# Kernel optimization log

Hardware: AMD Instinct MI355X
Metric: run time of the kernel (lower is better)

The kernel has to match this reference:

```python
import jax, jax.numpy as jnp
import numpy as np

N_NODES = 65536   # N
D_HID   = 128     # D (hidden)
N_GROUPS = 16384  # G portfolios
GROUP_LEN = 64    # lines per portfolio (port_len entries)
N_LINES = N_GROUPS * GROUP_LEN  # L
BATCH = 16384     # B samples


def setup_inputs() -> dict:
    key = jax.random.key(0)
    k = jax.random.split(key, 5)
    H = jax.random.normal(k[0], (N_NODES, D_HID), dtype=jnp.float32)
    port_w_signed_flat = jax.random.normal(k[1], (N_LINES,), dtype=jnp.float32)
    anchor_idx = jax.random.randint(k[2], (BATCH,), 0, N_NODES, dtype=jnp.int32)
    pf_gid = jax.random.randint(k[3], (BATCH,), 0, N_GROUPS, dtype=jnp.int32)
    port_nodes_flat = jax.random.randint(k[4], (N_LINES,), 0, N_NODES, dtype=jnp.int32)
    port_len = jnp.full((N_GROUPS,), GROUP_LEN, dtype=jnp.int32)
    return {
        'H': H,
        'port_w_signed_flat': port_w_signed_flat,
        'anchor_idx': anchor_idx,
        'pf_gid': pf_gid,
        'port_nodes_flat': port_nodes_flat,
        'port_len': port_len,
    }


def reference(H, port_w_signed_flat, anchor_idx, pf_gid, port_nodes_flat, port_len):
    """Faithful, vectorized port of compute_samplewise_portfolio_vectors_loo.

    Ragged segment-weighted mean per portfolio group, with strict leave-one-out
    correction for each sample's anchor node, followed by L2 normalization.
    Returns (V_abs, V_sgn), each [B, D].
    """
    N, D = H.shape
    G = port_len.shape[0]
    L = port_nodes_flat.shape[0]

    # gid per flat line: repeat_interleave(arange(G), lens)
    gid_lines = jnp.repeat(jnp.arange(G, dtype=jnp.int32), port_len,
                           total_repeat_length=L)

    w_abs = jnp.abs(port_w_signed_flat)
    Hl = H[port_nodes_flat]                                  # [L, D] gather
    S_abs = jax.ops.segment_sum(w_abs[:, None] * Hl, gid_lines, num_segments=G)
    W_abs = jax.ops.segment_sum(w_abs, gid_lines, num_segments=G)
    W_sgn = jax.ops.segment_sum(port_w_signed_flat, gid_lines, num_segments=G)

    valid = (pf_gid >= 0) & (pf_gid < G)
    g = jnp.clip(pf_gid, 0, G - 1)

    # Leave-one-out self-weight: sum of w over lines where (gid==g_i, node==anchor_i).
    # Vectorized join via a sorted composite int32 key (G*N < 2^31 by construction).
    keys_l = gid_lines * N + port_nodes_flat                 # [L]
    keys_s = g * N + anchor_idx                              # [B]
    order = jnp.argsort(keys_l)
    sk = keys_l[order]
    zero1 = jnp.zeros((1,), H.dtype)
    ca = jnp.concatenate([zero1, jnp.cumsum(w_abs[order])])
    cs = jnp.concatenate([zero1, jnp.cumsum(port_w_signed_flat[order])])
    lo = jnp.searchsorted(sk, keys_s, side='left')
    hi = jnp.searchsorted(sk, keys_s, side='right')
    self_w_abs = ca[hi] - ca[lo]                             # [B]
    self_w_sgn = cs[hi] - cs[lo]                             # [B]

    Ha = H[anchor_idx]                                       # [B, D]
    denom = jnp.maximum(W_abs[g] - self_w_abs, 1e-12)        # clamp_min
    V_abs = (S_abs[g] - self_w_abs[:, None] * Ha) / denom[:, None]
    V_sgn = ((W_sgn[g] - self_w_sgn) / denom)[:, None] * V_abs

    V_abs = jnp.where(valid[:, None], V_abs, jnp.zeros((), H.dtype))
    V_sgn = jnp.where(valid[:, None], V_sgn, jnp.zeros((), H.dtype))

    # torch F.normalize: x / clamp(||x||, min=eps)
    na = jnp.linalg.norm(V_abs, axis=1, keepdims=True)
    V_abs = V_abs / jnp.maximum(na, 1e-6)
    ns = jnp.linalg.norm(V_sgn, axis=1, keepdims=True)
    V_sgn = jnp.where(ns > 0, V_sgn / jnp.maximum(ns, 1e-6), V_sgn)
    return V_abs, V_sgn
```

## Files before the change

### kernel.cpp

```cpp
#include <hip/hip_runtime.h>
#include <hip/hip_bf16.h>


__global__ __launch_bounds__(1024) void scan_offsets_kernel(
    const int* __restrict__ len, int* __restrict__ offs, int G) {
    __shared__ int part[1024];
    const int t = threadIdx.x;
    const int chunk = (G + 1023) >> 10;
    const int lo = min(t * chunk, G);
    const int hi = min(lo + chunk, G);
    int s = 0;
    for (int i = lo; i < hi; ++i) s += len[i];
    part[t] = s;
    __syncthreads();
    #pragma unroll
    for (int ofs = 1; ofs < 1024; ofs <<= 1) {
        int v = (t >= ofs) ? part[t - ofs] : 0;
        __syncthreads();
        part[t] += v;
        __syncthreads();
    }
    int run = part[t] - s;
    for (int i = lo; i < hi; ++i) { offs[i] = run; run += len[i]; }
}

__global__ __launch_bounds__(256) void pf_loo_kernel(
    const float* __restrict__ H,
    const float* __restrict__ pw,
    const int* __restrict__ anchor_idx,
    const int* __restrict__ pf_gid,
    const int* __restrict__ pn,
    const int* __restrict__ plen,
    const int* __restrict__ offs,
    float* __restrict__ out,
    int B, int G) {
    const int b = blockIdx.x * (blockDim.x >> 6) + (threadIdx.x >> 6);
    const int lane = threadIdx.x & 63;
    const int half = lane >> 5;
    const int qlane = lane & 31;
    if (b >= B) return;

    float4* outA = (float4*)(out + (size_t)b * 128);
    float4* outS = (float4*)(out + ((size_t)B + b) * 128);

    const int gid = pf_gid[b];
    if (!(gid >= 0 && gid < G)) {
        float4 z = make_float4(0.f, 0.f, 0.f, 0.f);
        if (half == 0) { outA[qlane] = z; outS[qlane] = z; }
        return;
    }

    const int anchor = anchor_idx[b];
    const int off = offs[gid];
    const int len = plen[gid];

    float4 acc = make_float4(0.f, 0.f, 0.f, 0.f);
    float laWa = 0.f, laWs = 0.f, laSa = 0.f, laSs = 0.f;

    for (int base = 0; base < len; base += 64) {
        const int jmax = min(64, len - base);
        float wl = 0.f;
        int nl = 0;
        if (lane < jmax) {
            wl = pw[off + base + lane];
            nl = pn[off + base + lane];
        }
        const float wla = fabsf(wl);
        laWa += wla;
        laWs += wl;
        if (nl == anchor && lane < jmax) { laSa += wla; laSs += wl; }

        #pragma unroll 8
        for (int jj = 0; jj < 64; jj += 2) {
            const float w0 = __shfl(wl, jj);
            const float w1 = __shfl(wl, jj + 1);
            const int n0 = __shfl(nl, jj);
            const int n1 = __shfl(nl, jj + 1);
            const int row = half ? n1 : n0;
            const float ww = fabsf(half ? w1 : w0);
            const float4 h = ((const float4*)(H + (size_t)row * 128))[qlane];
            acc.x = fmaf(ww, h.x, acc.x);
            acc.y = fmaf(ww, h.y, acc.y);
            acc.z = fmaf(ww, h.z, acc.z);
            acc.w = fmaf(ww, h.w, acc.w);
        }
    }

    #pragma unroll
    for (int m = 32; m; m >>= 1) {
        laWa += __shfl_xor(laWa, m);
        laWs += __shfl_xor(laWs, m);
        laSa += __shfl_xor(laSa, m);
        laSs += __shfl_xor(laSs, m);
    }
    acc.x += __shfl_xor(acc.x, 32);
    acc.y += __shfl_xor(acc.y, 32);
    acc.z += __shfl_xor(acc.z, 32);
    acc.w += __shfl_xor(acc.w, 32);

    const float denom = fmaxf(laWa - laSa, 1e-12f);
    const float4 hv = ((const float4*)(H + (size_t)anchor * 128))[qlane];

    float4 v;
    v.x = (acc.x - laSa * hv.x) / denom;
    v.y = (acc.y - laSa * hv.y) / denom;
    v.z = (acc.z - laSa * hv.z) / denom;
    v.w = (acc.w - laSa * hv.w) / denom;
    const float scale = (laWs - laSs) / denom;

    float n2 = v.x * v.x + v.y * v.y + v.z * v.z + v.w * v.w;
    #pragma unroll
    for (int m = 32; m; m >>= 1) n2 += __shfl_xor(n2, m);
    n2 *= 0.5f;
    const float na = sqrtf(n2);

    const float invA = 1.0f / fmaxf(na, 1e-6f);
    const float ns = fabsf(scale) * na;
    const float sgnscale = (ns > 0.f) ? (scale / fmaxf(ns, 1e-6f)) : scale;

    const float s = half ? sgnscale : invA;
    float4 res;
    res.x = v.x * s; res.y = v.y * s; res.z = v.z * s; res.w = v.w * s;
    float4* dst = half ? outS : outA;
    dst[qlane] = res;
}

extern "C" void kernel_launch(void* const* d_in, const int* in_sizes, int n_in,
                              void* d_out, int out_size, void* d_ws, size_t ws_size,
                              hipStream_t stream) {
    const float* H      = (const float*)d_in[0];
    const float* pw     = (const float*)d_in[1];
    const int* anchor   = (const int*)d_in[2];
    const int* gid      = (const int*)d_in[3];
    const int* pn       = (const int*)d_in[4];
    const int* plen     = (const int*)d_in[5];
    float* out          = (float*)d_out;

    const int B = in_sizes[2];
    const int G = in_sizes[5];

    int* offs = (int*)d_ws;

    scan_offsets_kernel<<<1, 1024, 0, stream>>>(plen, offs, G);

    const int wavesPerBlock = 4;
    const int blocks = (B + wavesPerBlock - 1) / wavesPerBlock;
    pf_loo_kernel<<<blocks, 256, 0, stream>>>(H, pw, anchor, gid, pn, plen,
                                              offs, out, B, G);
}
```

Measured before the change: 172.4 us.

## Gather H from a bf16 copy with four rows per wave step

Adds a pre-pass that converts H to bf16 with round-to-nearest-even into the workspace. The main kernel then gathers 16-byte bf16 chunks, so each wave covers four portfolio rows per step instead of two, with 8 fp32 accumulators per lane. The goal is to halve the bytes moved by the random row gather, which dominates the kernel. In exchange it adds a full read and write of H on every call and lowers input precision, and it falls back to the fp32 path when the workspace is too small.

Measured after the change: 147.3 us. -14.6%, faster.

```diff
diff --git a/kernel.cpp b/kernel.cpp
--- a/kernel.cpp
+++ b/kernel.cpp
@@ -24,20 +24,40 @@
     for (int i = lo; i < hi; ++i) { offs[i] = run; run += len[i]; }
 }
 
-__global__ __launch_bounds__(256) void pf_loo_kernel(
-    const float* __restrict__ H,
+__device__ inline unsigned bf_rne(float x) {
+    unsigned u = __float_as_uint(x);
+    return (u + 0x7FFFu + ((u >> 16) & 1u)) >> 16;
+}
+
+__global__ __launch_bounds__(256) void convert_h_kernel(
+    const float4* __restrict__ H4, uint2* __restrict__ Hb, int n4) {
+    const int i = blockIdx.x * blockDim.x + threadIdx.x;
+    if (i >= n4) return;
+    const float4 v = H4[i];
+    uint2 o;
+    o.x = bf_rne(v.x) | (bf_rne(v.y) << 16);
+    o.y = bf_rne(v.z) | (bf_rne(v.w) << 16);
+    Hb[i] = o;
+}
+
+__device__ inline void unpack2(unsigned d, float& lo, float& hi) {
+    lo = __uint_as_float(d << 16);
+    hi = __uint_as_float(d & 0xFFFF0000u);
+}
+
+__global__ __launch_bounds__(256) void pf_loo_bf16(
+    const unsigned short* __restrict__ Hb,
     const float* __restrict__ pw,
     const int* __restrict__ anchor_idx,
     const int* __restrict__ pf_gid,
     const int* __restrict__ pn,
     const int* __restrict__ plen,
     const int* __restrict__ offs,
-    float* __restrict__ out,
-    int B, int G) {
+    float* __restrict__ out, int B, int G) {
     const int b = blockIdx.x * (blockDim.x >> 6) + (threadIdx.x >> 6);
     const int lane = threadIdx.x & 63;
-    const int half = lane >> 5;
-    const int qlane = lane & 31;
+    const int q = lane >> 4;
+    const int s = lane & 15;
     if (b >= B) return;
 
     float4* outA = (float4*)(out + (size_t)b * 128);
@@ -45,8 +65,9 @@
 
     const int gid = pf_gid[b];
     if (!(gid >= 0 && gid < G)) {
-        float4 z = make_float4(0.f, 0.f, 0.f, 0.f);
-        if (half == 0) { outA[qlane] = z; outS[qlane] = z; }
+        const float4 z = make_float4(0.f, 0.f, 0.f, 0.f);
+        if (q == 0) { outA[2 * s] = z; outA[2 * s + 1] = z; }
+        if (q == 1) { outS[2 * s] = z; outS[2 * s + 1] = z; }
         return;
     }
 
@@ -54,7 +75,7 @@
     const int off = offs[gid];
     const int len = plen[gid];
 
-    float4 acc = make_float4(0.f, 0.f, 0.f, 0.f);
+    float acc[8] = {0.f, 0.f, 0.f, 0.f, 0.f, 0.f, 0.f, 0.f};
     float laWa = 0.f, laWs = 0.f, laSa = 0.f, laSs = 0.f;
 
     for (int base = 0; base < len; base += 64) {
@@ -68,16 +89,113 @@
         const float wla = fabsf(wl);
         laWa += wla;
         laWs += wl;
-        if (nl == anchor && lane < jmax) { laSa += wla; laSs += wl; }
-
+        if (nl == anchor) { laSa += wla; laSs += wl; }
+
+        #pragma unroll 8
+        for (int jj = 0; jj < 64; jj += 4) {
+            const float ww = fabsf(__shfl(wl, jj + q));
+            const int row = __shfl(nl, jj + q);
+            const uint4 h = *((const uint4*)(Hb + (size_t)row * 128) + s);
+            float f0, f1, f2, f3, f4, f5, f6, f7;
+            unpack2(h.x, f0, f1);
+            unpack2(h.y, f2, f3);
+            unpack2(h.z, f4, f5);
+            unpack2(h.w, f6, f7);
+            acc[0] = fmaf(ww, f0, acc[0]);
+            acc[1] = fmaf(ww, f1, acc[1]);
+            acc[2] = fmaf(ww, f2, acc[2]);
+            acc[3] = fmaf(ww, f3, acc[3]);
+            acc[4] = fmaf(ww, f4, acc[4]);
+            acc[5] = fmaf(ww, f5, acc[5]);
+            acc[6] = fmaf(ww, f6, acc[6]);
+            acc[7] = fmaf(ww, f7, acc[7]);
+        }
+    }
+
+    #pragma unroll
+    for (int m = 32; m; m >>= 1) {
+        laWa += __shfl_xor(laWa, m);
+        laWs += __shfl_xor(laWs, m);
+        laSa += __shfl_xor(laSa, m);
+        laSs += __shfl_xor(laSs, m);
+    }
+    #pragma unroll
+    for (int k = 0; k < 8; ++k) {
+        acc[k] += __shfl_xor(acc[k], 16);
+        acc[k] += __shfl_xor(acc[k], 32);
+    }
+
+    const float denom = fmaxf(laWa - laSa, 1e-12f);
+    const uint4 ha = *((const uint4*)(Hb + (size_t)anchor * 128) + s);
+    float h0, h1, h2, h3, h4, h5, h6, h7;
+    unpack2(ha.x, h0, h1);
+    unpack2(ha.y, h2, h3);
+    unpack2(ha.z, h4, h5);
+    unpack2(ha.w, h6, h7);
+    const float hv[8] = {h0, h1, h2, h3, h4, h5, h6, h7};
+
+    float v[8];
+    float n2 = 0.f;
+    #pragma unroll
+    for (int k = 0; k < 8; ++k) {
+        v[k] = (acc[k] - laSa * hv[k]) / denom;
+        n2 = fmaf(v[k], v[k], n2);
+    }
+    const float scale = (laWs - laSs) / denom;
+
+    #pragma unroll
+    for (int m = 32; m; m >>= 1) n2 += __shfl_xor(n2, m);
+    n2 *= 0.25f;
+    const float na = sqrtf(n2);
+
+    const float invA = 1.0f / fmaxf(na, 1e-6f);
+    const float ns = fabsf(scale) * na;
+    const float sgnscale = (ns > 0.f) ? (scale / fmaxf(ns, 1e-6f)) : scale;
+
+    if (q == 0) {
+        outA[2 * s] = make_float4(v[0] * invA, v[1] * invA, v[2] * invA, v[3] * invA);
+        outA[2 * s + 1] = make_float4(v[4] * invA, v[5] * invA, v[6] * invA, v[7] * invA);
+    } else if (q == 1) {
+        outS[2 * s] = make_float4(v[0] * sgnscale, v[1] * sgnscale, v[2] * sgnscale, v[3] * sgnscale);
+        outS[2 * s + 1] = make_float4(v[4] * sgnscale, v[5] * sgnscale, v[6] * sgnscale, v[7] * sgnscale);
+    }
+}
+
+__global__ __launch_bounds__(256) void pf_loo_f32(
+    const float* __restrict__ H, const float* __restrict__ pw,
+    const int* __restrict__ anchor_idx, const int* __restrict__ pf_gid,
+    const int* __restrict__ pn, const int* __restrict__ plen,
+    const int* __restrict__ offs, float* __restrict__ out, int B, int G) {
+    const int b = blockIdx.x * (blockDim.x >> 6) + (threadIdx.x >> 6);
+    const int lane = threadIdx.x & 63;
+    const int half = lane >> 5;
+    const int qlane = lane & 31;
+    if (b >= B) return;
+    float4* outA = (float4*)(out + (size_t)b * 128);
+    float4* outS = (float4*)(out + ((size_t)B + b) * 128);
+    const int gid = pf_gid[b];
+    if (!(gid >= 0 && gid < G)) {
+        float4 z = make_float4(0.f, 0.f, 0.f, 0.f);
+        if (half == 0) { outA[qlane] = z; outS[qlane] = z; }
+        return;
+    }
+    const int anchor = anchor_idx[b];
+    const int off = offs[gid];
+    const int len = plen[gid];
+    float4 acc = make_float4(0.f, 0.f, 0.f, 0.f);
+    float laWa = 0.f, laWs = 0.f, laSa = 0.f, laSs = 0.f;
+    for (int base = 0; base < len; base += 64) {
+        const int jmax = min(64, len - base);
+        float wl = 0.f;
+        int nl = 0;
+        if (lane < jmax) { wl = pw[off + base + lane]; nl = pn[off + base + lane]; }
+        const float wla = fabsf(wl);
+        laWa += wla; laWs += wl;
+        if (nl == anchor) { laSa += wla; laSs += wl; }
         #pragma unroll 8
         for (int jj = 0; jj < 64; jj += 2) {
-            const float w0 = __shfl(wl, jj);
-            const float w1 = __shfl(wl, jj + 1);
-            const int n0 = __shfl(nl, jj);
-            const int n1 = __shfl(nl, jj + 1);
-            const int row = half ? n1 : n0;
-            const float ww = fabsf(half ? w1 : w0);
+            const float ww = fabsf(__shfl(wl, jj + half));
+            const int row = __shfl(nl, jj + half);
             const float4 h = ((const float4*)(H + (size_t)row * 128))[qlane];
             acc.x = fmaf(ww, h.x, acc.x);
             acc.y = fmaf(ww, h.y, acc.y);
@@ -85,7 +203,6 @@
             acc.w = fmaf(ww, h.w, acc.w);
         }
     }
-
     #pragma unroll
     for (int m = 32; m; m >>= 1) {
         laWa += __shfl_xor(laWa, m);
@@ -97,30 +214,24 @@
     acc.y += __shfl_xor(acc.y, 32);
     acc.z += __shfl_xor(acc.z, 32);
     acc.w += __shfl_xor(acc.w, 32);
-
     const float denom = fmaxf(laWa - laSa, 1e-12f);
     const float4 hv = ((const float4*)(H + (size_t)anchor * 128))[qlane];
-
     float4 v;
     v.x = (acc.x - laSa * hv.x) / denom;
     v.y = (acc.y - laSa * hv.y) / denom;
     v.z = (acc.z - laSa * hv.z) / denom;
     v.w = (acc.w - laSa * hv.w) / denom;
     const float scale = (laWs - laSs) / denom;
-
     float n2 = v.x * v.x + v.y * v.y + v.z * v.z + v.w * v.w;
     #pragma unroll
     for (int m = 32; m; m >>= 1) n2 += __shfl_xor(n2, m);
     n2 *= 0.5f;
     const float na = sqrtf(n2);
-
     const float invA = 1.0f / fmaxf(na, 1e-6f);
     const float ns = fabsf(scale) * na;
     const float sgnscale = (ns > 0.f) ? (scale / fmaxf(ns, 1e-6f)) : scale;
-
-    const float s = half ? sgnscale : invA;
-    float4 res;
-    res.x = v.x * s; res.y = v.y * s; res.z = v.z * s; res.w = v.w * s;
+    const float sc = half ? sgnscale : invA;
+    float4 res = make_float4(v.x * sc, v.y * sc, v.z * sc, v.w * sc);
     float4* dst = half ? outS : outA;
     dst[qlane] = res;
 }
@@ -138,13 +249,25 @@
 
     const int B = in_sizes[2];
     const int G = in_sizes[5];
-
-    int* offs = (int*)d_ws;
-
-    scan_offsets_kernel<<<1, 1024, 0, stream>>>(plen, offs, G);
+    const int ND = in_sizes[0];
+    const size_t hb_bytes = (size_t)ND * 2;
 
     const int wavesPerBlock = 4;
     const int blocks = (B + wavesPerBlock - 1) / wavesPerBlock;
-    pf_loo_kernel<<<blocks, 256, 0, stream>>>(H, pw, anchor, gid, pn, plen,
-                                              offs, out, B, G);
-}
+
+    if (ws_size >= hb_bytes + (size_t)G * 4) {
+        unsigned short* Hb = (unsigned short*)d_ws;
+        int* offsp = (int*)((char*)d_ws + hb_bytes);
+        const int n4 = ND / 4;
+        convert_h_kernel<<<(n4 + 255) / 256, 256, 0, stream>>>(
+            (const float4*)H, (uint2*)Hb, n4);
+        scan_offsets_kernel<<<1, 1024, 0, stream>>>(plen, offsp, G);
+        pf_loo_bf16<<<blocks, 256, 0, stream>>>(Hb, pw, anchor, gid, pn, plen,
+                                                offsp, out, B, G);
+    } else {
+        int* offsp = (int*)d_ws;
+        scan_offsets_kernel<<<1, 1024, 0, stream>>>(plen, offsp, G);
+        pf_loo_f32<<<blocks, 256, 0, stream>>>(H, pw, anchor, gid, pn, plen,
+                                               offsp, out, B, G);
+    }
+}
```
